# Performance work log

Measured on AMD Instinct MI355X. Metric: run time of the kernel, lower is better.

Reference implementation:

```python
import jax, jax.numpy as jnp
import numpy as np

BN_EPS = 1e-5


def setup_inputs() -> dict:
    key = jax.random.key(0)
    ks = jax.random.split(key, 14)
    B, N, C, NS = 2, 1024, 512, 64
    seed_xyz = jax.random.uniform(ks[0], (B, N, 3), jnp.float32)          # points in unit cube
    seed_features = jax.random.normal(ks[1], (B, C, N), jnp.float32)
    # per-seed rotation matrices (orthonormalized via QR)
    rot = jnp.linalg.qr(jax.random.normal(ks[2], (B, N, 3, 3), jnp.float32))[0]
    # cuboid extents sized so each query finds a reasonable neighbor count
    crop_size = 0.2 + 0.3 * jax.random.uniform(ks[3], (B, N, 3), jnp.float32)
    W1 = jax.random.normal(ks[4], (256, 3 + C), jnp.float32) / np.float32(np.sqrt(3 + C))
    gamma1 = 1.0 + 0.1 * jax.random.normal(ks[5], (256,), jnp.float32)
    beta1 = 0.1 * jax.random.normal(ks[6], (256,), jnp.float32)
    mean1 = 0.1 * jax.random.normal(ks[7], (256,), jnp.float32)
    var1 = 0.5 + jax.random.uniform(ks[8], (256,), jnp.float32)
    W2 = jax.random.normal(ks[9], (256, 256), jnp.float32) / np.float32(16.0)
    gamma2 = 1.0 + 0.1 * jax.random.normal(ks[10], (256,), jnp.float32)
    beta2 = 0.1 * jax.random.normal(ks[11], (256,), jnp.float32)
    mean2 = 0.1 * jax.random.normal(ks[12], (256,), jnp.float32)
    var2 = 0.5 + jax.random.uniform(ks[13], (256,), jnp.float32)
    return dict(seed_xyz=seed_xyz, seed_features=seed_features, rot=rot,
                crop_size=crop_size, W1=W1, gamma1=gamma1, beta1=beta1,
                mean1=mean1, var1=var1, W2=W2, gamma2=gamma2, beta2=beta2,
                mean2=mean2, var2=var2, nsample=NS)


def _conv_bn_relu(x, W, g, b, m, v):
    # 1x1 conv (no bias, bn=True) + inference BatchNorm + ReLU
    y = jnp.einsum('bpnc,oc->bpno', x, W)
    scale = g * jax.lax.rsqrt(v + BN_EPS)
    return jax.nn.relu((y - m) * scale + b)


def reference(seed_xyz, seed_features, rot, crop_size,
              W1, gamma1, beta1, mean1, var1,
              W2, gamma2, beta2, mean2, var2, nsample):
    # ---- rotated rectangular query + group (queries == points == seed_xyz) ----
    # diff[b,p,n] = xyz[b,n] - query[b,p]; rotate into the query's local frame
    diff = seed_xyz[:, None, :, :] - seed_xyz[:, :, None, :]          # (B,P,N,3)
    local = jnp.einsum('bpnj,bpjk->bpnk', diff, rot)                  # (B,P,N,3)
    inside = jnp.all(jnp.abs(local) <= 0.5 * crop_size[:, :, None, :], axis=-1)  # (B,P,N)
    # first `nsample` in-region indices, invalid slots filled with the first hit
    order = jnp.argsort(jnp.where(inside, 0, 1).astype(jnp.int32), axis=-1, stable=True)
    idx = order[..., :nsample]                                        # (B,P,NS)
    valid = jnp.take_along_axis(inside, idx, axis=-1)
    idx = jnp.where(valid, idx, idx[..., :1])
    # gather rotated local xyz and features
    g_xyz = jnp.take_along_axis(local, idx[..., None], axis=2)        # (B,P,NS,3)
    feats = jnp.swapaxes(seed_features, 1, 2)                         # (B,N,C)
    g_feat = jax.vmap(lambda f, i: f[i])(feats, idx)                  # (B,P,NS,C)
    grouped = jnp.concatenate([g_xyz, g_feat], axis=-1)               # (B,P,NS,3+C)
    # ---- SharedMLP (1x1 conv + BN + ReLU) x2, then max over samples ----
    h = _conv_bn_relu(grouped, W1, gamma1, beta1, mean1, var1)
    h = _conv_bn_relu(h, W2, gamma2, beta2, mean2, var2)
    out = jnp.max(h, axis=2)                                          # (B,P,256)
    return jnp.swapaxes(out, 1, 2)                                    # (B,256,P)
```

## Files before the change

### kernel.cpp

```cpp
#include <hip/hip_runtime.h>
#include <hip/hip_bf16.h>
#include <math.h>

typedef __attribute__((ext_vector_type(8))) __bf16 bf16x8;
typedef __attribute__((ext_vector_type(4))) __bf16 bf16x4;
typedef __attribute__((ext_vector_type(2))) __bf16 bf16x2;
typedef __attribute__((ext_vector_type(4))) float f32x4;

#define NPTS 1024
#define CIN 512
#define NSAMP 64
#define LDFT 520
#define LDFO 136

__device__ __forceinline__ void local_coords(const float* q, float cx, float cy, float cz,
                                             const float R[9], float& l0, float& l1, float& l2) {
    float d0 = __fsub_rn(q[0], cx);
    float d1 = __fsub_rn(q[1], cy);
    float d2 = __fsub_rn(q[2], cz);
    l0 = __fadd_rn(__fadd_rn(__fmul_rn(d0, R[0]), __fmul_rn(d1, R[3])), __fmul_rn(d2, R[6]));
    l1 = __fadd_rn(__fadd_rn(__fmul_rn(d0, R[1]), __fmul_rn(d1, R[4])), __fmul_rn(d2, R[7]));
    l2 = __fadd_rn(__fadd_rn(__fmul_rn(d0, R[2]), __fmul_rn(d1, R[5])), __fmul_rn(d2, R[8]));
}

__global__ void prep_kernel(const float* __restrict__ W1, const float* __restrict__ W2,
                            const float* __restrict__ g1, const float* __restrict__ be1,
                            const float* __restrict__ m1, const float* __restrict__ v1,
                            const float* __restrict__ g2, const float* __restrict__ be2,
                            const float* __restrict__ m2, const float* __restrict__ v2,
                            __bf16* __restrict__ W1f, __bf16* __restrict__ W2s,
                            float* __restrict__ wxs,
                            float* __restrict__ s1, float* __restrict__ b1,
                            float* __restrict__ s2, float* __restrict__ b2) {
    const int o = blockIdx.x;
    const int t = threadIdx.x;
    if (t == 0) {
        float sc1 = g1[o] / sqrtf(v1[o] + 1e-5f);
        s1[o] = sc1;
        b1[o] = be1[o] - m1[o] * sc1;
        float sc2 = g2[o] / sqrtf(v2[o] + 1e-5f);
        s2[o] = sc2;
        b2[o] = be2[o] - m2[o] * sc2;
        wxs[o * 4 + 0] = sc1 * W1[o * 515 + 0];
        wxs[o * 4 + 1] = sc1 * W1[o * 515 + 1];
        wxs[o * 4 + 2] = sc1 * W1[o * 515 + 2];
        wxs[o * 4 + 3] = 0.f;
    }
    for (int k = t; k < CIN; k += blockDim.x)
        W1f[o * CIN + k] = (__bf16)W1[o * 515 + 3 + k];
    {
        const int f = o * 256 + t;
        const int j = f & 7;
        const int l = (f >> 3) & 63;
        const int nt = (f >> 9) & 3;
        const int ks = (f >> 11) & 7;
        const int w = (f >> 14) & 3;
        const int o2 = w * 64 + nt * 16 + (l & 15);
        const int k = ks * 32 + ((l >> 4) << 3) + j;
        W2s[f] = (__bf16)W2[o2 * 256 + k];
    }
}

__global__ __launch_bounds__(256) void select_kernel(const float* __restrict__ xyz,
                                                     const float* __restrict__ rot,
                                                     const float* __restrict__ crop,
                                                     unsigned short* __restrict__ seln_g) {
    __shared__ unsigned long long msk[16];
    __shared__ int wpre[17];
    __shared__ int selr[NSAMP];

    const int bid = blockIdx.x;
    const int b = bid >> 10;
    const int t = threadIdx.x;
    const int l = t & 63, w = t >> 6;

    const float cx = xyz[bid * 3 + 0], cy = xyz[bid * 3 + 1], cz = xyz[bid * 3 + 2];
    float R[9];
#pragma unroll
    for (int j = 0; j < 9; ++j) R[j] = rot[bid * 9 + j];
    const float h0 = 0.5f * crop[bid * 3 + 0];
    const float h1 = 0.5f * crop[bid * 3 + 1];
    const float h2 = 0.5f * crop[bid * 3 + 2];

#pragma unroll
    for (int i = 0; i < 4; ++i) {
        const int n = i * 256 + t;
        float l0, l1, l2;
        local_coords(xyz + (size_t)(b * NPTS + n) * 3, cx, cy, cz, R, l0, l1, l2);
        bool ins = (__builtin_fabsf(l0) <= h0) && (__builtin_fabsf(l1) <= h1) &&
                   (__builtin_fabsf(l2) <= h2);
        unsigned long long bal = __ballot(ins);
        if (l == 0) msk[i * 4 + w] = bal;
    }
    __syncthreads();
    if (t < 64) {
        const int c = (t < 16) ? __popcll(msk[t]) : 0;
        int sum = c;
#pragma unroll
        for (int d = 1; d < 16; d <<= 1) {
            int v = __shfl_up(sum, d);
            if (t >= d) sum += v;
        }
        if (t < 16) wpre[t] = sum - c;
        if (t == 15) wpre[16] = sum;
    }
    __syncthreads();
    const int cnt = wpre[16];
#pragma unroll
    for (int i = 0; i < 4; ++i) {
        const int n = i * 256 + t;
        const unsigned long long wd = msk[n >> 6];
        const int bit = n & 63;
        if ((wd >> bit) & 1ull) {
            int rank = wpre[n >> 6] + __popcll(wd & ((1ull << bit) - 1ull));
            if (rank < NSAMP) selr[rank] = n;
        }
    }
    __syncthreads();
    if (t < NSAMP) {
        const int n = (t < cnt) ? selr[t] : selr[0];
        seln_g[bid * NSAMP + t] = (unsigned short)n;
    }
}

__global__ __launch_bounds__(256) void fgemm_kernel(const float* __restrict__ feats,
                                                    const __bf16* __restrict__ W1f,
                                                    const float* __restrict__ s1,
                                                    const float* __restrict__ b1,
                                                    __bf16* __restrict__ Fsb) {
    __shared__ __align__(16) __bf16 Ft[16][LDFT];
    __shared__ __align__(16) __bf16 Fo[16][LDFO];
    const int t = threadIdx.x;
    const int b = blockIdx.x >> 7;
    const int half = (blockIdx.x >> 6) & 1;
    const int n0 = (blockIdx.x & 63) << 4;
    const int l = t & 63, w = t >> 6;
    const int lo = l & 15, kg = l >> 4;

    const float* fb = feats + (size_t)b * (CIN * NPTS) + n0;

    {
        const int n = t & 15;
        const int cq = (t >> 4) * 2;
        for (int i = 0; i < 16; ++i) {
            int c = i * 32 + cq;
            float v0 = fb[(size_t)c * NPTS + n];
            float v1 = fb[(size_t)(c + 1) * NPTS + n];
            bf16x2 pk = {(__bf16)v0, (__bf16)v1};
            *(bf16x2*)(&Ft[n][c]) = pk;
        }
    }
    __syncthreads();

    f32x4 acc[2];
#pragma unroll
    for (int mt = 0; mt < 2; ++mt) acc[mt] = f32x4{0.f, 0.f, 0.f, 0.f};

#pragma unroll
    for (int ks = 0; ks < 16; ++ks) {
        const int kk = ks * 32 + kg * 8;
        const bf16x8 bfr = *(const bf16x8*)(&Ft[lo][kk]);
#pragma unroll
        for (int mt = 0; mt < 2; ++mt) {
            const int o = half * 128 + w * 32 + mt * 16 + lo;
            const bf16x8 af = *(const bf16x8*)(&W1f[(size_t)o * CIN + kk]);
            acc[mt] = __builtin_amdgcn_mfma_f32_16x16x32_bf16(af, bfr, acc[mt], 0, 0, 0);
        }
    }
    __syncthreads();
#pragma unroll
    for (int mt = 0; mt < 2; ++mt) {
        const int ol = w * 32 + mt * 16 + kg * 4;
        const f32x4 sv = *(const f32x4*)(&s1[half * 128 + ol]);
        const f32x4 bv = *(const f32x4*)(&b1[half * 128 + ol]);
        bf16x4 r;
#pragma unroll
        for (int j = 0; j < 4; ++j) r[j] = (__bf16)fmaf(acc[mt][j], sv[j], bv[j]);
        *(bf16x4*)(&Fo[lo][ol]) = r;
    }
    __syncthreads();
    {
        const int row = t >> 4, c = t & 15;
        const bf16x8 v = *(const bf16x8*)(&Fo[row][c * 8]);
        *(bf16x8*)(&Fsb[((size_t)(b * NPTS + n0 + row)) * 256 + half * 128 + c * 8]) = v;
    }
}

__global__ __launch_bounds__(256, 4) void fused_kernel(
    const float* __restrict__ xyz, const float* __restrict__ rot,
    const __bf16* __restrict__ Fsb, const float* __restrict__ wxs,
    const unsigned short* __restrict__ seln_g,
    const __bf16* __restrict__ W2s, const float* __restrict__ s2g, const float* __restrict__ b2g,
    float* __restrict__ out) {
    __shared__ __align__(16) char A2raw[NSAMP * 512];
    __shared__ __align__(16) f32x4 lc[NSAMP];
    __shared__ int seln_l[NSAMP];

    const int bid = ((int)blockIdx.x & 7) * 256 + ((int)blockIdx.x >> 3);
    const int b = bid >> 10;
    const int p = bid & 1023;
    const int t = threadIdx.x;
    const int l = t & 63, w = t >> 6;
    const int lo = l & 15, kg = l >> 4;

    const int oc = (t & 31) * 8;
    f32x4 wv[8];
#pragma unroll
    for (int j = 0; j < 8; ++j) wv[j] = *(const f32x4*)(&wxs[(oc + j) * 4]);

    if (t < NSAMP) {
        const int n = (int)seln_g[bid * NSAMP + t];
        seln_l[t] = n;
        const float cx = xyz[bid * 3 + 0], cy = xyz[bid * 3 + 1], cz = xyz[bid * 3 + 2];
        float R[9];
#pragma unroll
        for (int j = 0; j < 9; ++j) R[j] = rot[bid * 9 + j];
        float l0, l1, l2;
        local_coords(xyz + (size_t)(b * NPTS + n) * 3, cx, cy, cz, R, l0, l1, l2);
        lc[t] = f32x4{l0, l1, l2, 0.f};
    }
    __syncthreads();

    {
        const int sgrp = t >> 5;
#pragma unroll
        for (int si = 0; si < 8; ++si) {
            const int s = sgrp * 8 + si;
            const f32x4 cd = lc[s];
            const bf16x8 fv = *(const bf16x8*)(&Fsb[((size_t)(b * NPTS + seln_l[s])) * 256 + oc]);
            bf16x8 pk;
#pragma unroll
            for (int j = 0; j < 8; ++j) {
                const float fj = (float)fv[j];
                const float x = fmaf(cd.x, wv[j].x, fmaf(cd.y, wv[j].y, fmaf(cd.z, wv[j].z, fj)));
                pk[j] = (__bf16)fmaxf(x, 0.f);
            }
            *(bf16x8*)(A2raw + s * 512 + ((oc * 2) ^ ((s & 7) << 4))) = pk;
        }
    }
    __syncthreads();

    f32x4 acc[4][4];
#pragma unroll
    for (int mt = 0; mt < 4; ++mt)
#pragma unroll
        for (int nt = 0; nt < 4; ++nt)
            acc[mt][nt] = f32x4{0.f, 0.f, 0.f, 0.f};

    const int ob = w * 64;
#pragma unroll
    for (int ks = 0; ks < 8; ++ks) {
        const int kkb = ks * 64 + kg * 16;
        bf16x8 af[4];
#pragma unroll
        for (int mt = 0; mt < 4; ++mt) {
            const int row = mt * 16 + lo;
            af[mt] = *(const bf16x8*)(A2raw + row * 512 + (kkb ^ ((row & 7) << 4)));
        }
#pragma unroll
        for (int nt = 0; nt < 4; ++nt) {
            const bf16x8 bfr = *(const bf16x8*)(&W2s[(size_t)(((w * 8 + ks) * 4 + nt)) * 512 + l * 8]);
#pragma unroll
            for (int mt = 0; mt < 4; ++mt)
                acc[mt][nt] = __builtin_amdgcn_mfma_f32_16x16x32_bf16(af[mt], bfr, acc[mt][nt], 0, 0, 0);
        }
    }

#pragma unroll
    for (int nt = 0; nt < 4; ++nt) {
        const int o = ob + nt * 16 + lo;
        const float sc = s2g[o], bb = b2g[o];
        float mx = 0.f;
#pragma unroll
        for (int mt = 0; mt < 4; ++mt)
#pragma unroll
            for (int r = 0; r < 4; ++r)
                mx = fmaxf(mx, fmaxf(fmaf(acc[mt][nt][r], sc, bb), 0.f));
        mx = fmaxf(mx, __shfl_xor(mx, 16));
        mx = fmaxf(mx, __shfl_xor(mx, 32));
        if (kg == 0)
            out[(size_t)b * (256 * NPTS) + (size_t)o * NPTS + p] = mx;
    }
}

extern "C" void kernel_launch(void* const* d_in, const int* in_sizes, int n_in,
                              void* d_out, int out_size, void* d_ws, size_t ws_size,
                              hipStream_t stream) {
    (void)in_sizes; (void)n_in; (void)out_size; (void)ws_size;
    const float* xyz   = (const float*)d_in[0];
    const float* feats = (const float*)d_in[1];
    const float* rot   = (const float*)d_in[2];
    const float* crop  = (const float*)d_in[3];
    const float* W1    = (const float*)d_in[4];
    const float* g1    = (const float*)d_in[5];
    const float* be1   = (const float*)d_in[6];
    const float* m1    = (const float*)d_in[7];
    const float* v1    = (const float*)d_in[8];
    const float* W2    = (const float*)d_in[9];
    const float* g2    = (const float*)d_in[10];
    const float* be2   = (const float*)d_in[11];
    const float* m2    = (const float*)d_in[12];
    const float* v2    = (const float*)d_in[13];

    char* ws = (char*)d_ws;
    __bf16* W1f = (__bf16*)(ws + 0);
    __bf16* W2s = (__bf16*)(ws + 262144);
    float*  wxs = (float*)(ws + 393216);
    float*  s1  = (float*)(ws + 397312);
    float*  b1  = (float*)(ws + 398336);
    float*  s2  = (float*)(ws + 399360);
    float*  b2  = (float*)(ws + 400384);
    __bf16* Fsb = (__bf16*)(ws + 401408);
    unsigned short* seln = (unsigned short*)(ws + 1449984);

    prep_kernel<<<256, 256, 0, stream>>>(W1, W2, g1, be1, m1, v1, g2, be2, m2, v2,
                                         W1f, W2s, wxs, s1, b1, s2, b2);
    select_kernel<<<2048, 256, 0, stream>>>(xyz, rot, crop, seln);
    fgemm_kernel<<<256, 256, 0, stream>>>(feats, W1f, s1, b1, Fsb);
    fused_kernel<<<2048, 256, 0, stream>>>(xyz, rot, Fsb, wxs, seln, W2s, s2, b2,
                                           (float*)d_out);
}
```

Before: 45.97 us.

## Process four queries per block with register-resident W2 and prefetched gathers

The fused kernel now uses 512-thread blocks that each handle four consecutive query points. Each wave keeps its W2 fragments in registers across all four points, and the feature gather for the next point is issued before the current point's MFMA. Outputs are staged in shared memory and written as contiguous 4-float vectors. The prep and select kernels are merged into one launch. This cuts repeated W2 loads, launch count and scattered output stores, at the cost of higher register pressure and fewer blocks.

```diff
diff --git a/kernel.cpp b/kernel.cpp
--- a/kernel.cpp
+++ b/kernel.cpp
@@ -23,55 +23,55 @@
     l2 = __fadd_rn(__fadd_rn(__fmul_rn(d0, R[2]), __fmul_rn(d1, R[5])), __fmul_rn(d2, R[8]));
 }
 
-__global__ void prep_kernel(const float* __restrict__ W1, const float* __restrict__ W2,
-                            const float* __restrict__ g1, const float* __restrict__ be1,
-                            const float* __restrict__ m1, const float* __restrict__ v1,
-                            const float* __restrict__ g2, const float* __restrict__ be2,
-                            const float* __restrict__ m2, const float* __restrict__ v2,
-                            __bf16* __restrict__ W1f, __bf16* __restrict__ W2s,
-                            float* __restrict__ wxs,
-                            float* __restrict__ s1, float* __restrict__ b1,
-                            float* __restrict__ s2, float* __restrict__ b2) {
-    const int o = blockIdx.x;
-    const int t = threadIdx.x;
-    if (t == 0) {
-        float sc1 = g1[o] / sqrtf(v1[o] + 1e-5f);
-        s1[o] = sc1;
-        b1[o] = be1[o] - m1[o] * sc1;
-        float sc2 = g2[o] / sqrtf(v2[o] + 1e-5f);
-        s2[o] = sc2;
-        b2[o] = be2[o] - m2[o] * sc2;
-        wxs[o * 4 + 0] = sc1 * W1[o * 515 + 0];
-        wxs[o * 4 + 1] = sc1 * W1[o * 515 + 1];
-        wxs[o * 4 + 2] = sc1 * W1[o * 515 + 2];
-        wxs[o * 4 + 3] = 0.f;
-    }
-    for (int k = t; k < CIN; k += blockDim.x)
-        W1f[o * CIN + k] = (__bf16)W1[o * 515 + 3 + k];
-    {
-        const int f = o * 256 + t;
-        const int j = f & 7;
-        const int l = (f >> 3) & 63;
-        const int nt = (f >> 9) & 3;
-        const int ks = (f >> 11) & 7;
-        const int w = (f >> 14) & 3;
-        const int o2 = w * 64 + nt * 16 + (l & 15);
-        const int k = ks * 32 + ((l >> 4) << 3) + j;
-        W2s[f] = (__bf16)W2[o2 * 256 + k];
-    }
-}
-
-__global__ __launch_bounds__(256) void select_kernel(const float* __restrict__ xyz,
-                                                     const float* __restrict__ rot,
-                                                     const float* __restrict__ crop,
-                                                     unsigned short* __restrict__ seln_g) {
+__global__ __launch_bounds__(256) void setup_kernel(
+    const float* __restrict__ xyz, const float* __restrict__ rot,
+    const float* __restrict__ crop,
+    const float* __restrict__ W1, const float* __restrict__ W2,
+    const float* __restrict__ g1, const float* __restrict__ be1,
+    const float* __restrict__ m1, const float* __restrict__ v1,
+    const float* __restrict__ g2, const float* __restrict__ be2,
+    const float* __restrict__ m2, const float* __restrict__ v2,
+    __bf16* __restrict__ W1f, __bf16* __restrict__ W2s,
+    float* __restrict__ wxs,
+    float* __restrict__ s1, float* __restrict__ b1,
+    float* __restrict__ s2, float* __restrict__ b2,
+    unsigned short* __restrict__ seln_g) {
     __shared__ unsigned long long msk[16];
     __shared__ int wpre[17];
     __shared__ int selr[NSAMP];
 
-    const int bid = blockIdx.x;
+    const int t = threadIdx.x;
+    if (blockIdx.x < 256) {
+        const int o = blockIdx.x;
+        if (t == 0) {
+            float sc1 = g1[o] / sqrtf(v1[o] + 1e-5f);
+            s1[o] = sc1;
+            b1[o] = be1[o] - m1[o] * sc1;
+            float sc2 = g2[o] / sqrtf(v2[o] + 1e-5f);
+            s2[o] = sc2;
+            b2[o] = be2[o] - m2[o] * sc2;
+            wxs[o * 4 + 0] = sc1 * W1[o * 515 + 0];
+            wxs[o * 4 + 1] = sc1 * W1[o * 515 + 1];
+            wxs[o * 4 + 2] = sc1 * W1[o * 515 + 2];
+            wxs[o * 4 + 3] = 0.f;
+        }
+        for (int k = t; k < CIN; k += blockDim.x)
+            W1f[o * CIN + k] = (__bf16)W1[o * 515 + 3 + k];
+        {
+            const int f = o * 256 + t;
+            const int j = f & 7;
+            const int l = (f >> 3) & 63;
+            const int nt = (f >> 9) & 1;
+            const int ks = (f >> 10) & 7;
+            const int w = (f >> 13) & 7;
+            const int o2 = w * 32 + nt * 16 + (l & 15);
+            const int k = ks * 32 + ((l >> 4) << 3) + j;
+            W2s[f] = (__bf16)W2[o2 * 256 + k];
+        }
+        return;
+    }
+    const int bid = blockIdx.x - 256;
     const int b = bid >> 10;
-    const int t = threadIdx.x;
     const int l = t & 63, w = t >> 6;
 
     const float cx = xyz[bid * 3 + 0], cy = xyz[bid * 3 + 1], cz = xyz[bid * 3 + 2];
@@ -119,7 +119,7 @@
     __syncthreads();
     if (t < NSAMP) {
         const int n = (t < cnt) ? selr[t] : selr[0];
-        seln_g[bid * NSAMP + t] = (unsigned short)n;
+        seln_g[(size_t)bid * NSAMP + t] = (unsigned short)n;
     }
 }
 
@@ -186,100 +186,165 @@
     }
 }
 
-__global__ __launch_bounds__(256, 4) void fused_kernel(
+__global__ __launch_bounds__(512, 2) void fused_kernel(
     const float* __restrict__ xyz, const float* __restrict__ rot,
     const __bf16* __restrict__ Fsb, const float* __restrict__ wxs,
     const unsigned short* __restrict__ seln_g,
     const __bf16* __restrict__ W2s, const float* __restrict__ s2g, const float* __restrict__ b2g,
     float* __restrict__ out) {
     __shared__ __align__(16) char A2raw[NSAMP * 512];
-    __shared__ __align__(16) f32x4 lc[NSAMP];
-    __shared__ int seln_l[NSAMP];
-
-    const int bid = ((int)blockIdx.x & 7) * 256 + ((int)blockIdx.x >> 3);
-    const int b = bid >> 10;
-    const int p = bid & 1023;
+    __shared__ __align__(16) f32x4 lcb[NSAMP];
+    __shared__ __align__(16) float outst[256][4];
+
+    const int raw = (int)blockIdx.x;
+    const int pg = (raw & 7) * 64 + (raw >> 3);
+    const int b = pg >> 8;
+    const int p0 = (pg & 255) * 4;
     const int t = threadIdx.x;
     const int l = t & 63, w = t >> 6;
     const int lo = l & 15, kg = l >> 4;
 
+    bf16x8 wf[8][2];
+#pragma unroll
+    for (int ks = 0; ks < 8; ++ks)
+#pragma unroll
+        for (int nt = 0; nt < 2; ++nt)
+            wf[ks][nt] = *(const bf16x8*)(&W2s[(size_t)((((w * 8 + ks) * 2 + nt) * 64) + l) * 8]);
+
     const int oc = (t & 31) * 8;
+    const int sg = t >> 5;
     f32x4 wv[8];
 #pragma unroll
     for (int j = 0; j < 8; ++j) wv[j] = *(const f32x4*)(&wxs[(oc + j) * 4]);
 
-    if (t < NSAMP) {
-        const int n = (int)seln_g[bid * NSAMP + t];
-        seln_l[t] = n;
-        const float cx = xyz[bid * 3 + 0], cy = xyz[bid * 3 + 1], cz = xyz[bid * 3 + 2];
-        float R[9];
-#pragma unroll
-        for (int j = 0; j < 9; ++j) R[j] = rot[bid * 9 + j];
-        float l0, l1, l2;
-        local_coords(xyz + (size_t)(b * NPTS + n) * 3, cx, cy, cz, R, l0, l1, l2);
-        lc[t] = f32x4{l0, l1, l2, 0.f};
-    }
-    __syncthreads();
+    float sc[2], bb[2];
+#pragma unroll
+    for (int nt = 0; nt < 2; ++nt) {
+        const int o = w * 32 + nt * 16 + lo;
+        sc[nt] = s2g[o];
+        bb[nt] = b2g[o];
+    }
+
+    bf16x8 stg[4];
 
     {
-        const int sgrp = t >> 5;
-#pragma unroll
-        for (int si = 0; si < 8; ++si) {
-            const int s = sgrp * 8 + si;
-            const f32x4 cd = lc[s];
-            const bf16x8 fv = *(const bf16x8*)(&Fsb[((size_t)(b * NPTS + seln_l[s])) * 256 + oc]);
+        const int p = p0;
+        if (t < NSAMP) {
+            const int n = (int)seln_g[((size_t)(b * NPTS + p)) * 64 + t];
+            const int bid = b * NPTS + p;
+            const float cx = xyz[bid * 3 + 0], cy = xyz[bid * 3 + 1], cz = xyz[bid * 3 + 2];
+            float R[9];
+#pragma unroll
+            for (int j = 0; j < 9; ++j) R[j] = rot[bid * 9 + j];
+            float l0, l1, l2;
+            local_coords(xyz + (size_t)(b * NPTS + n) * 3, cx, cy, cz, R, l0, l1, l2);
+            lcb[t] = f32x4{l0, l1, l2, 0.f};
+        }
+#pragma unroll
+        for (int si = 0; si < 4; ++si) {
+            const int s = sg * 4 + si;
+            const int n = (int)seln_g[((size_t)(b * NPTS + p)) * 64 + s];
+            stg[si] = *(const bf16x8*)(&Fsb[((size_t)(b * NPTS + n)) * 256 + oc]);
+        }
+        __syncthreads();
+#pragma unroll
+        for (int si = 0; si < 4; ++si) {
+            const int s = sg * 4 + si;
+            const f32x4 cd = lcb[s];
             bf16x8 pk;
 #pragma unroll
             for (int j = 0; j < 8; ++j) {
-                const float fj = (float)fv[j];
-                const float x = fmaf(cd.x, wv[j].x, fmaf(cd.y, wv[j].y, fmaf(cd.z, wv[j].z, fj)));
+                const float x = fmaf(cd.x, wv[j].x,
+                                     fmaf(cd.y, wv[j].y, fmaf(cd.z, wv[j].z, (float)stg[si][j])));
                 pk[j] = (__bf16)fmaxf(x, 0.f);
             }
             *(bf16x8*)(A2raw + s * 512 + ((oc * 2) ^ ((s & 7) << 4))) = pk;
         }
-    }
-    __syncthreads();
-
-    f32x4 acc[4][4];
-#pragma unroll
-    for (int mt = 0; mt < 4; ++mt)
-#pragma unroll
-        for (int nt = 0; nt < 4; ++nt)
-            acc[mt][nt] = f32x4{0.f, 0.f, 0.f, 0.f};
-
-    const int ob = w * 64;
-#pragma unroll
-    for (int ks = 0; ks < 8; ++ks) {
-        const int kkb = ks * 64 + kg * 16;
-        bf16x8 af[4];
-#pragma unroll
-        for (int mt = 0; mt < 4; ++mt) {
-            const int row = mt * 16 + lo;
-            af[mt] = *(const bf16x8*)(A2raw + row * 512 + (kkb ^ ((row & 7) << 4)));
-        }
-#pragma unroll
-        for (int nt = 0; nt < 4; ++nt) {
-            const bf16x8 bfr = *(const bf16x8*)(&W2s[(size_t)(((w * 8 + ks) * 4 + nt)) * 512 + l * 8]);
+        __syncthreads();
+    }
+
+    for (int pi = 0; pi < 4; ++pi) {
+        if (pi < 3) {
+            const int p = p0 + pi + 1;
+            if (t < NSAMP) {
+                const int n = (int)seln_g[((size_t)(b * NPTS + p)) * 64 + t];
+                const int bid = b * NPTS + p;
+                const float cx = xyz[bid * 3 + 0], cy = xyz[bid * 3 + 1], cz = xyz[bid * 3 + 2];
+                float R[9];
+#pragma unroll
+                for (int j = 0; j < 9; ++j) R[j] = rot[bid * 9 + j];
+                float l0, l1, l2;
+                local_coords(xyz + (size_t)(b * NPTS + n) * 3, cx, cy, cz, R, l0, l1, l2);
+                lcb[t] = f32x4{l0, l1, l2, 0.f};
+            }
+#pragma unroll
+            for (int si = 0; si < 4; ++si) {
+                const int s = sg * 4 + si;
+                const int n = (int)seln_g[((size_t)(b * NPTS + p)) * 64 + s];
+                stg[si] = *(const bf16x8*)(&Fsb[((size_t)(b * NPTS + n)) * 256 + oc]);
+            }
+        }
+
+        f32x4 acc[4][2];
+#pragma unroll
+        for (int mt = 0; mt < 4; ++mt)
+#pragma unroll
+            for (int nt = 0; nt < 2; ++nt)
+                acc[mt][nt] = f32x4{0.f, 0.f, 0.f, 0.f};
+
+#pragma unroll
+        for (int ks = 0; ks < 8; ++ks) {
+            const int kkb = ks * 64 + kg * 16;
+            bf16x8 af[4];
+#pragma unroll
+            for (int mt = 0; mt < 4; ++mt) {
+                const int row = mt * 16 + lo;
+                af[mt] = *(const bf16x8*)(A2raw + row * 512 + (kkb ^ ((row & 7) << 4)));
+            }
+#pragma unroll
+            for (int nt = 0; nt < 2; ++nt)
+#pragma unroll
+                for (int mt = 0; mt < 4; ++mt)
+                    acc[mt][nt] = __builtin_amdgcn_mfma_f32_16x16x32_bf16(af[mt], wf[ks][nt],
+                                                                          acc[mt][nt], 0, 0, 0);
+        }
+
+#pragma unroll
+        for (int nt = 0; nt < 2; ++nt) {
+            float mx = 0.f;
 #pragma unroll
             for (int mt = 0; mt < 4; ++mt)
-                acc[mt][nt] = __builtin_amdgcn_mfma_f32_16x16x32_bf16(af[mt], bfr, acc[mt][nt], 0, 0, 0);
-        }
-    }
-
-#pragma unroll
-    for (int nt = 0; nt < 4; ++nt) {
-        const int o = ob + nt * 16 + lo;
-        const float sc = s2g[o], bb = b2g[o];
-        float mx = 0.f;
-#pragma unroll
-        for (int mt = 0; mt < 4; ++mt)
-#pragma unroll
-            for (int r = 0; r < 4; ++r)
-                mx = fmaxf(mx, fmaxf(fmaf(acc[mt][nt][r], sc, bb), 0.f));
-        mx = fmaxf(mx, __shfl_xor(mx, 16));
-        mx = fmaxf(mx, __shfl_xor(mx, 32));
-        if (kg == 0)
-            out[(size_t)b * (256 * NPTS) + (size_t)o * NPTS + p] = mx;
+#pragma unroll
+                for (int r = 0; r < 4; ++r)
+                    mx = fmaxf(mx, fmaxf(fmaf(acc[mt][nt][r], sc[nt], bb[nt]), 0.f));
+            mx = fmaxf(mx, __shfl_xor(mx, 16));
+            mx = fmaxf(mx, __shfl_xor(mx, 32));
+            if (kg == 0) outst[w * 32 + nt * 16 + lo][pi] = mx;
+        }
+        __syncthreads();
+
+        if (pi < 3) {
+#pragma unroll
+            for (int si = 0; si < 4; ++si) {
+                const int s = sg * 4 + si;
+                const f32x4 cd = lcb[s];
+                bf16x8 pk;
+#pragma unroll
+                for (int j = 0; j < 8; ++j) {
+                    const float x = fmaf(cd.x, wv[j].x,
+                                         fmaf(cd.y, wv[j].y, fmaf(cd.z, wv[j].z, (float)stg[si][j])));
+                    pk[j] = (__bf16)fmaxf(x, 0.f);
+                }
+                *(bf16x8*)(A2raw + s * 512 + ((oc * 2) ^ ((s & 7) << 4))) = pk;
+            }
+        }
+        __syncthreads();
+    }
+
+    if (t < 256) {
+        const int o = t;
+        const f32x4 v = *(const f32x4*)(&outst[o][0]);
+        *(f32x4*)(&out[((size_t)b * 256 + o) * NPTS + p0]) = v;
     }
 }
 
@@ -313,10 +378,10 @@
     __bf16* Fsb = (__bf16*)(ws + 401408);
     unsigned short* seln = (unsigned short*)(ws + 1449984);
 
-    prep_kernel<<<256, 256, 0, stream>>>(W1, W2, g1, be1, m1, v1, g2, be2, m2, v2,
-                                         W1f, W2s, wxs, s1, b1, s2, b2);
-    select_kernel<<<2048, 256, 0, stream>>>(xyz, rot, crop, seln);
+    setup_kernel<<<2304, 256, 0, stream>>>(xyz, rot, crop,
+                                           W1, W2, g1, be1, m1, v1, g2, be2, m2, v2,
+                                           W1f, W2s, wxs, s1, b1, s2, b2, seln);
     fgemm_kernel<<<256, 256, 0, stream>>>(feats, W1f, s1, b1, Fsb);
-    fused_kernel<<<2048, 256, 0, stream>>>(xyz, rot, Fsb, wxs, seln, W2s, s2, b2,
-                                           (float*)d_out);
-}
+    fused_kernel<<<512, 512, 0, stream>>>(xyz, rot, Fsb, wxs, seln, W2s, s2, b2,
+                                          (float*)d_out);
+}
```

Result: faster. 44.05 us (-4.2%).
